# Optimization experiments

Measured on AMD Instinct MI355X. Metric: run time of the kernel, lower is better.

Reference implementation:

```python
import jax, jax.numpy as jnp
import numpy as np
import math

B, S, D, H = 16, 512, 1024, 16
DH = D // H  # 64
NUM_DEG = 50
NUM_SPE = 512


def setup_inputs() -> dict:
    key = jax.random.key(0)
    ks = jax.random.split(key, 16)
    w = lambda k, shape: (jax.random.normal(k, shape, jnp.float32) * 0.02)
    return {
        "hidden_states": jax.random.normal(ks[0], (B, S, D), jnp.float32),
        "attention_mask": jnp.zeros((B, 1, 1, S), jnp.float32),
        "if_2d": 1,
        "in_degree": jax.random.randint(ks[1], (B, S), 0, NUM_DEG),
        "out_degree": jax.random.randint(ks[2], (B, S), 0, NUM_DEG),
        "spe": jax.random.randint(ks[3], (B, S, S), 0, NUM_SPE),
        "dist_3d": jax.random.normal(ks[4], (B, S), jnp.float32),
        "dist_m": jax.random.normal(ks[5], (B, S, S), jnp.float32),
        # Linear params stored as [in, out]; y = x @ W + b
        "Wq": w(ks[6], (D, D)), "bq": jnp.zeros((D,), jnp.float32),
        "Wk": w(ks[7], (D, D)), "bk": jnp.zeros((D,), jnp.float32),
        "Wv": w(ks[8], (D, D)), "bv": jnp.zeros((D,), jnp.float32),
        "W_in": w(ks[9], (NUM_DEG, D)),
        "W_out": w(ks[10], (NUM_DEG, D)),
        "W_spe": w(ks[11], (NUM_SPE, H)),
    }


def reference(hidden_states, attention_mask, if_2d, in_degree, out_degree,
              spe, dist_3d, dist_m, Wq, bq, Wk, bk, Wv, bv,
              W_in, W_out, W_spe):
    # if_2d == True branch (2D graph path). padding_idx=0 -> row 0 is zero.
    pad_mask = (jnp.arange(NUM_DEG) != 0).astype(hidden_states.dtype)[:, None]
    pos = (W_in * pad_mask)[in_degree] + (W_out * pad_mask)[out_degree]  # [B,S,D]
    bias = jnp.transpose(W_spe[spe], (0, 3, 1, 2))  # [B,S,S,H] -> [B,H,S,S]

    h = hidden_states + pos
    to_heads = lambda x: x.reshape(B, S, H, DH).transpose(0, 2, 1, 3)  # [B,H,S,DH]
    q = to_heads(h @ Wq + bq)
    k = to_heads(h @ Wk + bk)
    v = to_heads(h @ Wv + bv)

    scores = jnp.einsum('bhqd,bhkd->bhqk', q, k) / math.sqrt(DH)
    scores = scores + bias + attention_mask
    probs = jax.nn.softmax(scores, axis=-1)  # dropout p=0 (eval)
    ctx = jnp.einsum('bhqk,bhkd->bhqd', probs, v)  # [B,H,S,DH]
    ctx = ctx.transpose(0, 2, 1, 3).reshape(B, S, D)
    return ctx, probs
```

## Files before the change

kernel.cpp:

```cpp
#include <hip/hip_runtime.h>

#define Bc 16
#define Sc 512
#define Dc 1024
#define Hc 16
#define DHc 64

#define AS1 __attribute__((address_space(1)))
#define AS3 __attribute__((address_space(3)))

typedef __attribute__((ext_vector_type(8))) __bf16 bf16x8;
typedef __attribute__((ext_vector_type(4))) float f32x4;
typedef __attribute__((ext_vector_type(8))) unsigned short ushort8;

static __device__ __forceinline__ unsigned short f2bf(float f) {
  unsigned int u = __builtin_bit_cast(unsigned int, f);
  unsigned int r = (u + 0x7fffu + ((u >> 16) & 1u)) >> 16;
  return (unsigned short)r;
}
static __device__ __forceinline__ float bf2f(unsigned short u) {
  unsigned int x = ((unsigned int)u) << 16;
  return __builtin_bit_cast(float, x);
}

__global__ __launch_bounds__(256) void k_prep(
    const float* __restrict__ hidden, const int* __restrict__ ind,
    const int* __restrict__ outd, const float* __restrict__ Win,
    const float* __restrict__ Wout, const float* __restrict__ Wq,
    const float* __restrict__ Wk, const float* __restrict__ Wv,
    const float* __restrict__ Wspe, const int* __restrict__ spe,
    unsigned short* __restrict__ hbf, unsigned short* __restrict__ Wtq,
    unsigned short* __restrict__ Wtk, unsigned short* __restrict__ Wtv,
    float* __restrict__ WspeT, unsigned short* __restrict__ spe16) {
  __shared__ float tile[64][65];
  int blk = blockIdx.x;
  int t = threadIdx.x;
  if (blk < 8192) {
    int row = blk;
    int id = ind[row], od = outd[row];
    float fi = (id != 0) ? 1.f : 0.f;
    float fo = (od != 0) ? 1.f : 0.f;
    float4 a = ((const float4*)(hidden + (size_t)row * Dc))[t];
    float4 x = ((const float4*)(Win + (size_t)id * Dc))[t];
    float4 y = ((const float4*)(Wout + (size_t)od * Dc))[t];
    ushort4 r;
    r.x = f2bf(a.x + fi * x.x + fo * y.x);
    r.y = f2bf(a.y + fi * x.y + fo * y.y);
    r.z = f2bf(a.z + fi * x.z + fo * y.z);
    r.w = f2bf(a.w + fi * x.w + fo * y.w);
    ((ushort4*)(hbf + (size_t)row * Dc))[t] = r;
  } else if (blk < 8960) {
    int f = blk - 8192;
    int z = f >> 8, rem = f & 255;
    int ky = rem >> 4, nx = rem & 15;
    const float* W = z == 0 ? Wq : z == 1 ? Wk : Wv;
    unsigned short* Wt = z == 0 ? Wtq : z == 1 ? Wtk : Wtv;
    int k0 = ky * 64, n0 = nx * 64;
    int r = t >> 4, c4 = (t & 15) * 4;
    for (int rr = r; rr < 64; rr += 16) {
      float4 v = *(const float4*)(W + (size_t)(k0 + rr) * Dc + n0 + c4);
      tile[rr][c4 + 0] = v.x;
      tile[rr][c4 + 1] = v.y;
      tile[rr][c4 + 2] = v.z;
      tile[rr][c4 + 3] = v.w;
    }
    __syncthreads();
    for (int rr = r; rr < 64; rr += 16) {
      ushort4 o;
      o.x = f2bf(tile[c4 + 0][rr]);
      o.y = f2bf(tile[c4 + 1][rr]);
      o.z = f2bf(tile[c4 + 2][rr]);
      o.w = f2bf(tile[c4 + 3][rr]);
      *(ushort4*)(Wt + (size_t)(n0 + rr) * Dc + k0 + c4) = o;
    }
  } else if (blk < 8992) {
    int idx = (blk - 8960) * 256 + t;
    int h = idx >> 9, i = idx & 511;
    WspeT[idx] = Wspe[i * Hc + h];
  } else {
    size_t base = (size_t)(blk - 8992) * 2048 + t * 8;
    int4 a = *(const int4*)(spe + base);
    int4 c = *(const int4*)(spe + base + 4);
    ushort8 o;
    o[0] = (unsigned short)a.x; o[1] = (unsigned short)a.y;
    o[2] = (unsigned short)a.z; o[3] = (unsigned short)a.w;
    o[4] = (unsigned short)c.x; o[5] = (unsigned short)c.y;
    o[6] = (unsigned short)c.z; o[7] = (unsigned short)c.w;
    *(ushort8*)(spe16 + base) = o;
  }
}

__global__ __launch_bounds__(256) void k_gemm_mfma(
    const unsigned short* __restrict__ hbf,
    const unsigned short* __restrict__ Wtq, const float* __restrict__ bq,
    const unsigned short* __restrict__ Wtk, const float* __restrict__ bk,
    const unsigned short* __restrict__ Wtv, const float* __restrict__ bv,
    unsigned short* __restrict__ Qo, unsigned short* __restrict__ Ko,
    unsigned short* __restrict__ Vt) {
  int zsel = blockIdx.z;
  const unsigned short* Wt;
  const float* bias;
  if (zsel == 0) { Wt = Wtq; bias = bq; }
  else if (zsel == 1) { Wt = Wtk; bias = bk; }
  else { Wt = Wtv; bias = bv; }

  __shared__ __align__(16) unsigned short As0[128 * 32];
  __shared__ __align__(16) unsigned short As1[128 * 32];
  __shared__ __align__(16) unsigned short Bs0[128 * 32];
  __shared__ __align__(16) unsigned short Bs1[128 * 32];

  int tid = threadIdx.x, lane = tid & 63, wave = tid >> 6;
  int m0 = blockIdx.y * 128, n0 = blockIdx.x * 128;
  int wr = wave >> 1, wc = wave & 1;

  f32x4 acc[4][4] = {};

  int srow = lane >> 2;
  int skb = (lane & 3) * 8;
  const unsigned short* gA = hbf + (size_t)(m0 + srow) * Dc + skb;
  const unsigned short* gB = Wt + (size_t)(n0 + srow) * Dc + skb;

  int fr = lane & 15, kg = (lane >> 4) * 8;

  for (int k0 = 0; k0 < Dc; k0 += 64) {
#pragma unroll
    for (int cc = 0; cc < 2; ++cc) {
      int c = wave + cc * 4;
      __builtin_amdgcn_global_load_lds(
          (const AS1 void*)(gA + (size_t)c * 16 * Dc + k0),
          (AS3 void*)(As0 + c * 16 * 32), 16, 0, 0);
      __builtin_amdgcn_global_load_lds(
          (const AS1 void*)(gA + (size_t)c * 16 * Dc + k0 + 32),
          (AS3 void*)(As1 + c * 16 * 32), 16, 0, 0);
      __builtin_amdgcn_global_load_lds(
          (const AS1 void*)(gB + (size_t)c * 16 * Dc + k0),
          (AS3 void*)(Bs0 + c * 16 * 32), 16, 0, 0);
      __builtin_amdgcn_global_load_lds(
          (const AS1 void*)(gB + (size_t)c * 16 * Dc + k0 + 32),
          (AS3 void*)(Bs1 + c * 16 * 32), 16, 0, 0);
    }
    __syncthreads();

    bf16x8 af[4][2], bfr[4][2];
#pragma unroll
    for (int m = 0; m < 4; ++m) {
      af[m][0] = *(const bf16x8*)(As0 + (wr * 64 + m * 16 + fr) * 32 + kg);
      af[m][1] = *(const bf16x8*)(As1 + (wr * 64 + m * 16 + fr) * 32 + kg);
    }
#pragma unroll
    for (int n = 0; n < 4; ++n) {
      bfr[n][0] = *(const bf16x8*)(Bs0 + (wc * 64 + n * 16 + fr) * 32 + kg);
      bfr[n][1] = *(const bf16x8*)(Bs1 + (wc * 64 + n * 16 + fr) * 32 + kg);
    }
#pragma unroll
    for (int m = 0; m < 4; ++m)
#pragma unroll
      for (int n = 0; n < 4; ++n) {
        acc[m][n] = __builtin_amdgcn_mfma_f32_16x16x32_bf16(af[m][0], bfr[n][0], acc[m][n], 0, 0, 0);
        acc[m][n] = __builtin_amdgcn_mfma_f32_16x16x32_bf16(af[m][1], bfr[n][1], acc[m][n], 0, 0, 0);
      }
    __syncthreads();
  }

  int fq = lane >> 4;
  if (zsel < 2) {
    unsigned short* C = (zsel == 0) ? Qo : Ko;
    float scale = (zsel == 0) ? 0.125f : 1.f;
#pragma unroll
    for (int m = 0; m < 4; ++m) {
#pragma unroll
      for (int n = 0; n < 4; ++n) {
        int col = n0 + wc * 64 + n * 16 + fr;
        float bb = bias[col];
#pragma unroll
        for (int r = 0; r < 4; ++r) {
          int row = m0 + wr * 64 + m * 16 + fq * 4 + r;
          C[(size_t)row * Dc + col] = f2bf((acc[m][n][r] + bb) * scale);
        }
      }
    }
  } else {
#pragma unroll
    for (int m = 0; m < 4; ++m) {
#pragma unroll
      for (int n = 0; n < 4; ++n) {
        int col = n0 + wc * 64 + n * 16 + fr;
        int hh = col >> 6, dh = col & 63;
        float bb = bias[col];
        int row = m0 + wr * 64 + m * 16 + fq * 4;
        int bb_ = row >> 9, ss = row & 511;
        ushort4 pk;
        pk.x = f2bf(acc[m][n][0] + bb);
        pk.y = f2bf(acc[m][n][1] + bb);
        pk.z = f2bf(acc[m][n][2] + bb);
        pk.w = f2bf(acc[m][n][3] + bb);
        *(ushort4*)(Vt + ((size_t)(bb_ * Hc + hh) * DHc + dh) * Sc + ss) = pk;
      }
    }
  }
}

#define SWB 520
__global__ __launch_bounds__(256, 8) void k_attn(
    const unsigned short* __restrict__ Qb, const unsigned short* __restrict__ Kb,
    const unsigned short* __restrict__ Vt, const unsigned short* __restrict__ spe16,
    const float* __restrict__ WspeT, const float* __restrict__ mask,
    float* __restrict__ probs, float* __restrict__ ctx) {
  extern __shared__ char smem[];
  unsigned short* S = (unsigned short*)smem;
  float* Wb = (float*)(smem + 16640);
  float* Rinv = (float*)(smem + 16640 + 2048);

  int tid = threadIdx.x, lane = tid & 63, w = tid >> 6;
  int fr = lane & 15, fq = lane >> 4, kg8 = fq * 8;

  int flat = blockIdx.x;
  int xcd = flat & 7, idx = flat >> 3;
  int b = (idx >> 8) * 4 + (xcd >> 1);
  int h = (xcd & 1) * 8 + (idx & 7);
  int qt = (idx >> 3) & 31;
  int q0 = qt * 16;
  int rot = idx & 7;

  for (int i = tid; i < 512; i += 256) Wb[i] = WspeT[h * 512 + i];

  const unsigned short* spp0 =
      spe16 + (size_t)(b * Sc + q0 + w * 4) * Sc + lane * 8;
  ushort8 iv0 = *(const ushort8*)(spp0);
  ushort8 iv1 = *(const ushort8*)(spp0 + Sc);
  ushort8 iv2 = *(const ushort8*)(spp0 + 2 * Sc);
  ushort8 iv3 = *(const ushort8*)(spp0 + 3 * Sc);
  float4 mk0 = *(const float4*)(mask + b * Sc + lane * 8);
  float4 mk1 = *(const float4*)(mask + b * Sc + lane * 8 + 4);

  const unsigned short* qbase = Qb + (size_t)(b * Sc + q0) * Dc + h * DHc;
  bf16x8 af0 = *(const bf16x8*)(qbase + (size_t)fr * Dc + kg8);
  bf16x8 af1 = *(const bf16x8*)(qbase + (size_t)fr * Dc + 32 + kg8);

  const unsigned short* kptr =
      Kb + (size_t)(b * Sc + w * 16 + fr) * Dc + h * DHc;
  bf16x8 kfA0 = *(const bf16x8*)(kptr + (size_t)rot * 64 * Dc + kg8);
  bf16x8 kfA1 = *(const bf16x8*)(kptr + (size_t)rot * 64 * Dc + 32 + kg8);
#pragma unroll
  for (int i = 0; i < 8; ++i) {
    int it = (i + rot) & 7;
    bf16x8 kfB0, kfB1;
    if (i < 7) {
      int itn = (i + 1 + rot) & 7;
      const unsigned short* np = kptr + (size_t)itn * 64 * Dc;
      kfB0 = *(const bf16x8*)(np + kg8);
      kfB1 = *(const bf16x8*)(np + 32 + kg8);
    }
    f32x4 acc = {};
    __builtin_amdgcn_s_setprio(1);
    acc = __builtin_amdgcn_mfma_f32_16x16x32_bf16(kfA0, af0, acc, 0, 0, 0);
    acc = __builtin_amdgcn_mfma_f32_16x16x32_bf16(kfA1, af1, acc, 0, 0, 0);
    __builtin_amdgcn_s_setprio(0);
    ushort4 pk;
    pk.x = f2bf(acc[0]); pk.y = f2bf(acc[1]);
    pk.z = f2bf(acc[2]); pk.w = f2bf(acc[3]);
    *(ushort4*)(S + fr * SWB + it * 64 + w * 16 + fq * 4) = pk;
    kfA0 = kfB0; kfA1 = kfB1;
  }
  __syncthreads();

  {
#pragma unroll
    for (int r4 = 0; r4 < 4; ++r4) {
      int row = w * 4 + r4;
      ushort8 iv = (r4 == 0) ? iv0 : (r4 == 1) ? iv1 : (r4 == 2) ? iv2 : iv3;
      ushort8 sv = *(const ushort8*)(S + row * SWB + lane * 8);
      float e0 = __expf(bf2f(sv[0]) + Wb[iv[0]] + mk0.x);
      float e1 = __expf(bf2f(sv[1]) + Wb[iv[1]] + mk0.y);
      float e2 = __expf(bf2f(sv[2]) + Wb[iv[2]] + mk0.z);
      float e3 = __expf(bf2f(sv[3]) + Wb[iv[3]] + mk0.w);
      float e4 = __expf(bf2f(sv[4]) + Wb[iv[4]] + mk1.x);
      float e5 = __expf(bf2f(sv[5]) + Wb[iv[5]] + mk1.y);
      float e6 = __expf(bf2f(sv[6]) + Wb[iv[6]] + mk1.z);
      float e7 = __expf(bf2f(sv[7]) + Wb[iv[7]] + mk1.w);
      float sum = e0 + e1 + e2 + e3 + e4 + e5 + e6 + e7;
#pragma unroll
      for (int o = 32; o; o >>= 1) sum += __shfl_xor(sum, o);
      float rinv = 1.f / sum;
      ushort8 ev;
      ev[0] = f2bf(e0); ev[1] = f2bf(e1); ev[2] = f2bf(e2); ev[3] = f2bf(e3);
      ev[4] = f2bf(e4); ev[5] = f2bf(e5); ev[6] = f2bf(e6); ev[7] = f2bf(e7);
      *(ushort8*)(S + row * SWB + lane * 8) = ev;
      if (lane == 0) Rinv[row] = rinv;
    }
  }
  __syncthreads();

  const unsigned short* vptr =
      Vt + ((size_t)(b * Hc + h) * DHc + w * 16 + fr) * Sc;
  float* pbase = probs + (size_t)((b * Hc + h) * Sc + q0) * Sc;
  int prow_half = tid >> 7;
  int pcol = (tid & 127) * 4;
  f32x4 pacc0 = {}, pacc1 = {};
  bf16x8 vfA0 = *(const bf16x8*)(vptr + rot * 64 + kg8);
  bf16x8 vfA1 = *(const bf16x8*)(vptr + rot * 64 + 32 + kg8);
#pragma unroll
  for (int i = 0; i < 8; ++i) {
    int it = (i + rot) & 7;
    bf16x8 vfB0, vfB1;
    if (i < 7) {
      int itn = (i + 1 + rot) & 7;
      vfB0 = *(const bf16x8*)(vptr + itn * 64 + kg8);
      vfB1 = *(const bf16x8*)(vptr + itn * 64 + 32 + kg8);
    }
    {
      int row = i * 2 + prow_half;
      ushort4 sv = *(const ushort4*)(S + row * SWB + pcol);
      float rv = Rinv[row];
      f32x4 e;
      e[0] = bf2f(sv.x) * rv; e[1] = bf2f(sv.y) * rv;
      e[2] = bf2f(sv.z) * rv; e[3] = bf2f(sv.w) * rv;
      __builtin_nontemporal_store(e, (f32x4*)(pbase + (size_t)row * Sc + pcol));
    }
    bf16x8 pfr0 = *(const bf16x8*)(S + fr * SWB + it * 64 + kg8);
    bf16x8 pfr1 = *(const bf16x8*)(S + fr * SWB + it * 64 + 32 + kg8);
    __builtin_amdgcn_s_setprio(1);
    pacc0 = __builtin_amdgcn_mfma_f32_16x16x32_bf16(vfA0, pfr0, pacc0, 0, 0, 0);
    pacc1 = __builtin_amdgcn_mfma_f32_16x16x32_bf16(vfA1, pfr1, pacc1, 0, 0, 0);
    __builtin_amdgcn_s_setprio(0);
    vfA0 = vfB0; vfA1 = vfB1;
  }

  {
    float rv = Rinv[fr];
    f32x4 o;
    o[0] = (pacc0[0] + pacc1[0]) * rv;
    o[1] = (pacc0[1] + pacc1[1]) * rv;
    o[2] = (pacc0[2] + pacc1[2]) * rv;
    o[3] = (pacc0[3] + pacc1[3]) * rv;
    __builtin_nontemporal_store(
        o, (f32x4*)(ctx + (size_t)(b * Sc + q0 + fr) * Dc + h * DHc + w * 16 + fq * 4));
  }
}

extern "C" void kernel_launch(void* const* d_in, const int* in_sizes, int n_in,
                              void* d_out, int out_size, void* d_ws, size_t ws_size,
                              hipStream_t stream) {
  const float* hidden = (const float*)d_in[0];
  const float* amask = (const float*)d_in[1];
  const int* ind = (const int*)d_in[3];
  const int* outd = (const int*)d_in[4];
  const int* spe = (const int*)d_in[5];
  const float* Wq = (const float*)d_in[8];
  const float* bq = (const float*)d_in[9];
  const float* Wk = (const float*)d_in[10];
  const float* bk = (const float*)d_in[11];
  const float* Wv = (const float*)d_in[12];
  const float* bv = (const float*)d_in[13];
  const float* Win = (const float*)d_in[14];
  const float* Wout = (const float*)d_in[15];
  const float* Wspe = (const float*)d_in[16];

  char* ws = (char*)d_ws;
  const size_t BSD = (size_t)Bc * Sc * Dc;
  unsigned short* hbf = (unsigned short*)ws;
  unsigned short* Wtq = (unsigned short*)(ws + 16u * 1048576);
  unsigned short* Wtk = (unsigned short*)(ws + 18u * 1048576);
  unsigned short* Wtv = (unsigned short*)(ws + 20u * 1048576);
  float* WspeT = (float*)(ws + 22u * 1048576);
  unsigned short* Qb = (unsigned short*)(ws + 24u * 1048576);
  unsigned short* Kb = (unsigned short*)(ws + 40u * 1048576);
  unsigned short* Vt = (unsigned short*)(ws + 56u * 1048576);
  unsigned short* spe16 = (unsigned short*)(ws + 72u * 1048576);
  float* ctx = (float*)d_out;
  float* probs = (float*)d_out + BSD;

  (void)hipFuncSetAttribute((const void*)k_attn,
                            hipFuncAttributeMaxDynamicSharedMemorySize, 18752);

  k_prep<<<dim3(11040), 256, 0, stream>>>(hidden, ind, outd, Win, Wout, Wq, Wk,
                                          Wv, Wspe, spe, hbf, Wtq, Wtk, Wtv,
                                          WspeT, spe16);
  k_gemm_mfma<<<dim3(8, 64, 3), 256, 0, stream>>>(hbf, Wtq, bq, Wtk, bk, Wtv, bv, Qb, Kb, Vt);
  k_attn<<<dim3(8192), 256, 18752, stream>>>(Qb, Kb, Vt, spe16, WspeT, amask, probs, ctx);
}
```

Baseline: 227.7 us.

## Process 32 query rows per attention block to reuse K/V fragments

Each attention block now handles two 16-row query tiles (32 rows) instead of one. The loaded K and V fragments feed twice as many MFMAs, and the per-block head bias table load is amortized. The grid is halved, shared memory roughly doubles, and launch bounds drop to 4 blocks per CU. The spe index loads move from before the QK loop into the softmax loop, and the probs write is widened to 8 floats per lane. The cost is higher register and LDS use, lower occupancy and less latency hiding for the spe loads.

```diff
diff --git a/kernel.cpp b/kernel.cpp
--- a/kernel.cpp
+++ b/kernel.cpp
@@ -201,41 +201,39 @@
 }
 
 #define SWB 520
-__global__ __launch_bounds__(256, 8) void k_attn(
+__global__ __launch_bounds__(256, 4) void k_attn(
     const unsigned short* __restrict__ Qb, const unsigned short* __restrict__ Kb,
     const unsigned short* __restrict__ Vt, const unsigned short* __restrict__ spe16,
     const float* __restrict__ WspeT, const float* __restrict__ mask,
     float* __restrict__ probs, float* __restrict__ ctx) {
   extern __shared__ char smem[];
   unsigned short* S = (unsigned short*)smem;
-  float* Wb = (float*)(smem + 16640);
-  float* Rinv = (float*)(smem + 16640 + 2048);
+  float* Wb = (float*)(smem + 33280);
+  float* Rinv = (float*)(smem + 33280 + 2048);
 
   int tid = threadIdx.x, lane = tid & 63, w = tid >> 6;
   int fr = lane & 15, fq = lane >> 4, kg8 = fq * 8;
 
   int flat = blockIdx.x;
   int xcd = flat & 7, idx = flat >> 3;
-  int b = (idx >> 8) * 4 + (xcd >> 1);
+  int b = (idx >> 7) * 4 + (xcd >> 1);
   int h = (xcd & 1) * 8 + (idx & 7);
-  int qt = (idx >> 3) & 31;
-  int q0 = qt * 16;
+  int qt = (idx >> 3) & 15;
+  int q0 = qt * 32;
   int rot = idx & 7;
 
   for (int i = tid; i < 512; i += 256) Wb[i] = WspeT[h * 512 + i];
 
-  const unsigned short* spp0 =
-      spe16 + (size_t)(b * Sc + q0 + w * 4) * Sc + lane * 8;
-  ushort8 iv0 = *(const ushort8*)(spp0);
-  ushort8 iv1 = *(const ushort8*)(spp0 + Sc);
-  ushort8 iv2 = *(const ushort8*)(spp0 + 2 * Sc);
-  ushort8 iv3 = *(const ushort8*)(spp0 + 3 * Sc);
   float4 mk0 = *(const float4*)(mask + b * Sc + lane * 8);
   float4 mk1 = *(const float4*)(mask + b * Sc + lane * 8 + 4);
 
   const unsigned short* qbase = Qb + (size_t)(b * Sc + q0) * Dc + h * DHc;
-  bf16x8 af0 = *(const bf16x8*)(qbase + (size_t)fr * Dc + kg8);
-  bf16x8 af1 = *(const bf16x8*)(qbase + (size_t)fr * Dc + 32 + kg8);
+  bf16x8 af[2][2];
+#pragma unroll
+  for (int qh = 0; qh < 2; ++qh)
+#pragma unroll
+    for (int kk = 0; kk < 2; ++kk)
+      af[qh][kk] = *(const bf16x8*)(qbase + (size_t)(qh * 16 + fr) * Dc + kk * 32 + kg8);
 
   const unsigned short* kptr =
       Kb + (size_t)(b * Sc + w * 16 + fr) * Dc + h * DHc;
@@ -251,24 +249,31 @@
       kfB0 = *(const bf16x8*)(np + kg8);
       kfB1 = *(const bf16x8*)(np + 32 + kg8);
     }
-    f32x4 acc = {};
+    f32x4 acc0 = {}, acc1 = {};
     __builtin_amdgcn_s_setprio(1);
-    acc = __builtin_amdgcn_mfma_f32_16x16x32_bf16(kfA0, af0, acc, 0, 0, 0);
-    acc = __builtin_amdgcn_mfma_f32_16x16x32_bf16(kfA1, af1, acc, 0, 0, 0);
+    acc0 = __builtin_amdgcn_mfma_f32_16x16x32_bf16(kfA0, af[0][0], acc0, 0, 0, 0);
+    acc0 = __builtin_amdgcn_mfma_f32_16x16x32_bf16(kfA1, af[0][1], acc0, 0, 0, 0);
+    acc1 = __builtin_amdgcn_mfma_f32_16x16x32_bf16(kfA0, af[1][0], acc1, 0, 0, 0);
+    acc1 = __builtin_amdgcn_mfma_f32_16x16x32_bf16(kfA1, af[1][1], acc1, 0, 0, 0);
     __builtin_amdgcn_s_setprio(0);
-    ushort4 pk;
-    pk.x = f2bf(acc[0]); pk.y = f2bf(acc[1]);
-    pk.z = f2bf(acc[2]); pk.w = f2bf(acc[3]);
-    *(ushort4*)(S + fr * SWB + it * 64 + w * 16 + fq * 4) = pk;
+    ushort4 pk0, pk1;
+    pk0.x = f2bf(acc0[0]); pk0.y = f2bf(acc0[1]);
+    pk0.z = f2bf(acc0[2]); pk0.w = f2bf(acc0[3]);
+    pk1.x = f2bf(acc1[0]); pk1.y = f2bf(acc1[1]);
+    pk1.z = f2bf(acc1[2]); pk1.w = f2bf(acc1[3]);
+    *(ushort4*)(S + fr * SWB + it * 64 + w * 16 + fq * 4) = pk0;
+    *(ushort4*)(S + (16 + fr) * SWB + it * 64 + w * 16 + fq * 4) = pk1;
     kfA0 = kfB0; kfA1 = kfB1;
   }
   __syncthreads();
 
   {
-#pragma unroll
-    for (int r4 = 0; r4 < 4; ++r4) {
-      int row = w * 4 + r4;
-      ushort8 iv = (r4 == 0) ? iv0 : (r4 == 1) ? iv1 : (r4 == 2) ? iv2 : iv3;
+    const unsigned short* spp0 =
+        spe16 + (size_t)(b * Sc + q0 + w * 8) * Sc + lane * 8;
+#pragma unroll
+    for (int r8 = 0; r8 < 8; ++r8) {
+      int row = w * 8 + r8;
+      ushort8 iv = *(const ushort8*)(spp0 + (size_t)r8 * Sc);
       ushort8 sv = *(const ushort8*)(S + row * SWB + lane * 8);
       float e0 = __expf(bf2f(sv[0]) + Wb[iv[0]] + mk0.x);
       float e1 = __expf(bf2f(sv[1]) + Wb[iv[1]] + mk0.y);
@@ -294,9 +299,7 @@
   const unsigned short* vptr =
       Vt + ((size_t)(b * Hc + h) * DHc + w * 16 + fr) * Sc;
   float* pbase = probs + (size_t)((b * Hc + h) * Sc + q0) * Sc;
-  int prow_half = tid >> 7;
-  int pcol = (tid & 127) * 4;
-  f32x4 pacc0 = {}, pacc1 = {};
+  f32x4 pacc00 = {}, pacc01 = {}, pacc10 = {}, pacc11 = {};
   bf16x8 vfA0 = *(const bf16x8*)(vptr + rot * 64 + kg8);
   bf16x8 vfA1 = *(const bf16x8*)(vptr + rot * 64 + 32 + kg8);
 #pragma unroll
@@ -309,32 +312,43 @@
       vfB1 = *(const bf16x8*)(vptr + itn * 64 + 32 + kg8);
     }
     {
-      int row = i * 2 + prow_half;
-      ushort4 sv = *(const ushort4*)(S + row * SWB + pcol);
+      int row = i * 4 + w;
+      ushort8 sv = *(const ushort8*)(S + row * SWB + lane * 8);
       float rv = Rinv[row];
-      f32x4 e;
-      e[0] = bf2f(sv.x) * rv; e[1] = bf2f(sv.y) * rv;
-      e[2] = bf2f(sv.z) * rv; e[3] = bf2f(sv.w) * rv;
-      __builtin_nontemporal_store(e, (f32x4*)(pbase + (size_t)row * Sc + pcol));
-    }
-    bf16x8 pfr0 = *(const bf16x8*)(S + fr * SWB + it * 64 + kg8);
-    bf16x8 pfr1 = *(const bf16x8*)(S + fr * SWB + it * 64 + 32 + kg8);
+      f32x4 e0, e1;
+      e0[0] = bf2f(sv[0]) * rv; e0[1] = bf2f(sv[1]) * rv;
+      e0[2] = bf2f(sv[2]) * rv; e0[3] = bf2f(sv[3]) * rv;
+      e1[0] = bf2f(sv[4]) * rv; e1[1] = bf2f(sv[5]) * rv;
+      e1[2] = bf2f(sv[6]) * rv; e1[3] = bf2f(sv[7]) * rv;
+      float* pdst = pbase + (size_t)row * Sc + lane * 8;
+      __builtin_nontemporal_store(e0, (f32x4*)pdst);
+      __builtin_nontemporal_store(e1, (f32x4*)(pdst + 4));
+    }
+    bf16x8 p00 = *(const bf16x8*)(S + fr * SWB + it * 64 + kg8);
+    bf16x8 p01 = *(const bf16x8*)(S + fr * SWB + it * 64 + 32 + kg8);
+    bf16x8 p10 = *(const bf16x8*)(S + (16 + fr) * SWB + it * 64 + kg8);
+    bf16x8 p11 = *(const bf16x8*)(S + (16 + fr) * SWB + it * 64 + 32 + kg8);
     __builtin_amdgcn_s_setprio(1);
-    pacc0 = __builtin_amdgcn_mfma_f32_16x16x32_bf16(vfA0, pfr0, pacc0, 0, 0, 0);
-    pacc1 = __builtin_amdgcn_mfma_f32_16x16x32_bf16(vfA1, pfr1, pacc1, 0, 0, 0);
+    pacc00 = __builtin_amdgcn_mfma_f32_16x16x32_bf16(vfA0, p00, pacc00, 0, 0, 0);
+    pacc01 = __builtin_amdgcn_mfma_f32_16x16x32_bf16(vfA1, p01, pacc01, 0, 0, 0);
+    pacc10 = __builtin_amdgcn_mfma_f32_16x16x32_bf16(vfA0, p10, pacc10, 0, 0, 0);
+    pacc11 = __builtin_amdgcn_mfma_f32_16x16x32_bf16(vfA1, p11, pacc11, 0, 0, 0);
     __builtin_amdgcn_s_setprio(0);
     vfA0 = vfB0; vfA1 = vfB1;
   }
 
-  {
-    float rv = Rinv[fr];
+#pragma unroll
+  for (int qh = 0; qh < 2; ++qh) {
+    float rv = Rinv[qh * 16 + fr];
+    f32x4 a0 = (qh == 0) ? pacc00 : pacc10;
+    f32x4 a1 = (qh == 0) ? pacc01 : pacc11;
     f32x4 o;
-    o[0] = (pacc0[0] + pacc1[0]) * rv;
-    o[1] = (pacc0[1] + pacc1[1]) * rv;
-    o[2] = (pacc0[2] + pacc1[2]) * rv;
-    o[3] = (pacc0[3] + pacc1[3]) * rv;
+    o[0] = (a0[0] + a1[0]) * rv;
+    o[1] = (a0[1] + a1[1]) * rv;
+    o[2] = (a0[2] + a1[2]) * rv;
+    o[3] = (a0[3] + a1[3]) * rv;
     __builtin_nontemporal_store(
-        o, (f32x4*)(ctx + (size_t)(b * Sc + q0 + fr) * Dc + h * DHc + w * 16 + fq * 4));
+        o, (f32x4*)(ctx + (size_t)(b * Sc + q0 + qh * 16 + fr) * Dc + h * DHc + w * 16 + fq * 4));
   }
 }
 
@@ -371,11 +385,11 @@
   float* probs = (float*)d_out + BSD;
 
   (void)hipFuncSetAttribute((const void*)k_attn,
-                            hipFuncAttributeMaxDynamicSharedMemorySize, 18752);
+                            hipFuncAttributeMaxDynamicSharedMemorySize, 35456);
 
   k_prep<<<dim3(11040), 256, 0, stream>>>(hidden, ind, outd, Win, Wout, Wq, Wk,
                                           Wv, Wspe, spe, hbf, Wtq, Wtk, Wtv,
                                           WspeT, spe16);
   k_gemm_mfma<<<dim3(8, 64, 3), 256, 0, stream>>>(hbf, Wtq, bq, Wtk, bk, Wtv, bv, Qb, Kb, Vt);
-  k_attn<<<dim3(8192), 256, 18752, stream>>>(Qb, Kb, Vt, spe16, WspeT, amask, probs, ctx);
-}
+  k_attn<<<dim3(4096), 256, 35456, stream>>>(Qb, Kb, Vt, spe16, WspeT, amask, probs, ctx);
+}
```

Result: faster. 215.4 us (median of 2 runs) (-5.4%).
